# Kernel tuning notes

Measured on AMD Instinct MI355X. Metric: run time of the kernel, lower is better.

Reference implementation:

```python
import jax, jax.numpy as jnp
import numpy as np

B, S, D_MODEL, H, DK, DV, DOUT = 8, 2048, 1024, 1, 512, 512, 1024
EPS = 1e-6
TEMP = DK ** 0.5


def _ln(x, g, b):
    # LayerNorm over last dim, eps=1e-6, affine
    m = jnp.mean(x, axis=-1, keepdims=True)
    v = jnp.mean((x - m) ** 2, axis=-1, keepdims=True)
    return (x - m) * jax.lax.rsqrt(v + EPS) * g + b


def setup_inputs() -> dict:
    key = jax.random.key(0)
    ks = jax.random.split(key, 16)
    s = 0.02
    return {
        "q": jax.random.normal(ks[0], (B, S, D_MODEL), jnp.float32),
        "k": jax.random.normal(ks[1], (B, S, D_MODEL), jnp.float32),
        "v": jax.random.normal(ks[2], (B, S, D_MODEL), jnp.float32),
        "mask": jnp.ones((B, S, S), jnp.int32),
        "Wq": jax.random.normal(ks[3], (D_MODEL, H * DK), jnp.float32) * s,
        "bq": jnp.zeros((H * DK,), jnp.float32),
        "Wk": jax.random.normal(ks[4], (D_MODEL, H * DK), jnp.float32) * s,
        "bk": jnp.zeros((H * DK,), jnp.float32),
        "Wv": jax.random.normal(ks[5], (D_MODEL, H * DV), jnp.float32) * s,
        "bv": jnp.zeros((H * DV,), jnp.float32),
        "g_q": jnp.ones((H * DK,), jnp.float32),
        "be_q": jnp.zeros((H * DK,), jnp.float32),
        "g_k": jnp.ones((H * DK,), jnp.float32),
        "be_k": jnp.zeros((H * DK,), jnp.float32),
        "g_v": jnp.ones((H * DV,), jnp.float32),
        "be_v": jnp.zeros((H * DV,), jnp.float32),
        "W1": jax.random.normal(ks[6], (H * DV, H * DV), jnp.float32) * s,
        "b1": jnp.zeros((H * DV,), jnp.float32),
        "W2": jax.random.normal(ks[7], (H * DV, DOUT), jnp.float32) * s,
        "b2": jnp.zeros((DOUT,), jnp.float32),
    }


def reference(q, k, v, mask, Wq, bq, Wk, bk, Wv, bv, g_q, be_q, g_k, be_k, g_v, be_v, W1, b1, W2, b2):
    # QKV projections, viewed as (B, S, H, d)
    qp = (q @ Wq + bq).reshape(B, S, H, DK)
    kp = (k @ Wk + bk).reshape(B, S, H, DK)
    vp = (v @ Wv + bv).reshape(B, S, H, DV)
    residual = qp
    # per-(token,head) LayerNorm over last dim (valid only because H == 1 in source)
    qn = jnp.swapaxes(_ln(qp, g_q, be_q), 1, 2)  # (B, H, S, DK)
    kn = jnp.swapaxes(_ln(kp, g_k, be_k), 1, 2)
    vn = jnp.swapaxes(_ln(vp, g_v, be_v), 1, 2)
    # scaled dot-product attention with mask
    scores = jnp.einsum('bhqd,bhkd->bhqk', qn / TEMP, kn)
    scores = jnp.where(mask[:, None, :, :] == 0, -1e9, scores)
    attn = jax.nn.softmax(scores, axis=-1)
    out = jnp.einsum('bhqk,bhkd->bhqd', attn, vn)
    out = jnp.swapaxes(out, 1, 2).reshape(B, S, H * DV)
    # trailing 2-layer MLP
    out = jax.nn.relu(out @ W1 + b1) @ W2 + b2
    return (out, residual, jnp.squeeze(attn))
```

## Files before the change

kernel.cpp:

```cpp
#include <hip/hip_runtime.h>
#include <hip/hip_bf16.h>

typedef __attribute__((ext_vector_type(8))) short short8;
typedef __attribute__((ext_vector_type(4))) short short4v;
typedef __attribute__((ext_vector_type(4))) float f32x4;

#define INV_TEMP 0.044194173824159216f

__device__ __forceinline__ ushort f2bf(float f) {
  unsigned u = __float_as_uint(f);
  unsigned r = (u + 0x7FFFu + ((u >> 16) & 1u)) >> 16;
  return (ushort)r;
}
__device__ __forceinline__ float bf2f(ushort u) {
  union { unsigned i; float f; } x; x.i = ((unsigned)u) << 16; return x.f;
}

__device__ __forceinline__ void gload_lds16(const void* g, void* l) {
  __builtin_amdgcn_global_load_lds(
      (const __attribute__((address_space(1))) unsigned int*)(unsigned long long)(uintptr_t)g,
      (__attribute__((address_space(3))) unsigned int*)(unsigned)(uintptr_t)l,
      16, 0, 0);
}

__global__ __launch_bounds__(256)
void transpose_cvt_all(const float* __restrict__ Wq, const float* __restrict__ Wk,
                       const float* __restrict__ Wv, const float* __restrict__ W1,
                       const float* __restrict__ W2,
                       ushort* __restrict__ Tq, ushort* __restrict__ Tk,
                       ushort* __restrict__ Tv, ushort* __restrict__ T1,
                       ushort* __restrict__ T2) {
  const int z = blockIdx.z;
  const int K = (z < 3) ? 1024 : 512;
  const int N = (z == 4) ? 1024 : 512;
  if (blockIdx.x * 32 >= N || blockIdx.y * 32 >= K) return;
  const float* W = z == 0 ? Wq : (z == 1 ? Wk : (z == 2 ? Wv : (z == 3 ? W1 : W2)));
  ushort* WT = z == 0 ? Tq : (z == 1 ? Tk : (z == 2 ? Tv : (z == 3 ? T1 : T2)));
  __shared__ float tile[32][33];
  const int n0 = blockIdx.x * 32, k0 = blockIdx.y * 32;
  const int tx = threadIdx.x & 31, ty = threadIdx.x >> 5;
  #pragma unroll
  for (int i = ty; i < 32; i += 8)
    tile[i][tx] = W[(long)(k0 + i) * N + n0 + tx];
  __syncthreads();
  #pragma unroll
  for (int i = ty; i < 32; i += 8)
    WT[(long)(n0 + i) * K + k0 + tx] = f2bf(tile[tx][i]);
}

__global__ __launch_bounds__(256)
void transpose_bf16(const ushort* __restrict__ in, ushort* __restrict__ out, int S, int D) {
  __shared__ ushort tile[32][33];
  const ushort* inb = in + (long)blockIdx.z * S * D;
  ushort* outb = out + (long)blockIdx.z * S * D;
  const int d0 = blockIdx.x * 32, s0 = blockIdx.y * 32;
  const int tx = threadIdx.x & 31, ty = threadIdx.x >> 5;
  #pragma unroll
  for (int i = ty; i < 32; i += 8)
    tile[i][tx] = inb[(long)(s0 + i) * D + d0 + tx];
  __syncthreads();
  #pragma unroll
  for (int i = ty; i < 32; i += 8)
    outb[(long)(d0 + i) * S + s0 + tx] = tile[tx][i];
}

__global__ __launch_bounds__(256)
void ln3_kernel(const float* __restrict__ Xq, const ushort* __restrict__ Xk,
                const ushort* __restrict__ Xv,
                const float* __restrict__ gq, const float* __restrict__ beq,
                const float* __restrict__ gk, const float* __restrict__ bek,
                const float* __restrict__ gv, const float* __restrict__ bev,
                ushort* __restrict__ Oq, ushort* __restrict__ Ok, ushort* __restrict__ Ov) {
  const int which = blockIdx.y;
  const float* g = which == 0 ? gq : (which == 1 ? gk : gv);
  const float* be = which == 0 ? beq : (which == 1 ? bek : bev);
  ushort* out = which == 0 ? Oq : (which == 1 ? Ok : Ov);
  const float scale = which == 0 ? INV_TEMP : 1.0f;

  const int row = blockIdx.x * 4 + (threadIdx.x >> 6);
  const int lane = threadIdx.x & 63;
  f32x4 v0, v1;
  if (which == 0) {
    const float* x = Xq + (long)row * 512 + lane * 8;
    v0 = *(const f32x4*)x;
    v1 = *(const f32x4*)(x + 4);
  } else {
    const ushort* x = (which == 1 ? Xk : Xv) + (long)row * 512 + lane * 8;
    short8 vv = *(const short8*)x;
    #pragma unroll
    for (int j = 0; j < 4; j++) { v0[j] = bf2f((ushort)vv[j]); v1[j] = bf2f((ushort)vv[4 + j]); }
  }
  float s = v0[0]+v0[1]+v0[2]+v0[3]+v1[0]+v1[1]+v1[2]+v1[3];
  float ss = v0[0]*v0[0]+v0[1]*v0[1]+v0[2]*v0[2]+v0[3]*v0[3]
           + v1[0]*v1[0]+v1[1]*v1[1]+v1[2]*v1[2]+v1[3]*v1[3];
  #pragma unroll
  for (int off = 32; off; off >>= 1) { s += __shfl_xor(s, off); ss += __shfl_xor(ss, off); }
  const float mean = s * (1.0f/512.0f);
  const float var  = ss * (1.0f/512.0f) - mean*mean;
  const float rs = rsqrtf(var + 1e-6f);
  f32x4 g0 = *(const f32x4*)(g + lane*8);
  f32x4 g1 = *(const f32x4*)(g + lane*8 + 4);
  f32x4 b0 = *(const f32x4*)(be + lane*8);
  f32x4 b1 = *(const f32x4*)(be + lane*8 + 4);
  union { short8 v; ushort u[8]; } o;
  #pragma unroll
  for (int j = 0; j < 4; j++) o.u[j]     = f2bf(((v0[j]-mean)*rs*g0[j] + b0[j]) * scale);
  #pragma unroll
  for (int j = 0; j < 4; j++) o.u[4 + j] = f2bf(((v1[j]-mean)*rs*g1[j] + b1[j]) * scale);
  *(short8*)(out + (long)row * 512 + lane * 8) = o.v;
}

template<int EPI, bool HAS_BIAS, bool OUT_BF16, bool A_F32>
__global__ __launch_bounds__(256)
void gemm_tn_pipe(const void* __restrict__ Av, const ushort* __restrict__ Bt,
                  const float* __restrict__ bias, const int* __restrict__ maskp,
                  float* __restrict__ Cf, ushort* __restrict__ Cb,
                  float* __restrict__ partial,
                  const float* __restrict__ A2, const float* __restrict__ A3,
                  const ushort* __restrict__ Bt2, const ushort* __restrict__ Bt3,
                  const float* __restrict__ bias2, const float* __restrict__ bias3,
                  ushort* __restrict__ Cb2,
                  int M, int N, int K,
                  long sA, long sB, long sC) {
  __shared__ char smem_raw[66048];
  ushort (*As)[128 * 64] = (ushort(*)[128 * 64])smem_raw;
  ushort (*Bs)[128 * 64] = (ushort(*)[128 * 64])(smem_raw + 32768);
  float* zloc = (float*)(smem_raw + 65536);
  float* smf  = (float*)smem_raw;

  const int tid = threadIdx.x;
  const int lane = tid & 63;
  const int wave = tid >> 6;
  const int wr = wave >> 1;
  const int wc = wave & 1;

  const int gx = gridDim.x, gy = gridDim.y;
  int lin = blockIdx.x + gx * (blockIdx.y + gy * blockIdx.z);
  const int nwg = gx * gy * (int)gridDim.z;
  int swz = lin;
  if ((nwg & 7) == 0) {
    const int q8 = nwg >> 3;
    swz = (lin & 7) * q8 + (lin >> 3);
  }
  const int bx = swz % gx;
  const int tmp = swz / gx;
  const int by = tmp % gy;
  const int bz = tmp / gy;

  const long zb = bz;
  const float* Afp;
  const ushort* Bb;
  const float* bias_p = bias;
  if constexpr (EPI == 4) {
    Afp = (bz == 0 ? (const float*)Av : (bz == 1 ? A2 : A3)) + (long)by * 128 * K;
    Bb = (bz == 0 ? Bt : (bz == 1 ? Bt2 : Bt3)) + (long)bx * 128 * K;
    bias_p = bz == 0 ? bias : (bz == 1 ? bias2 : bias3);
  } else {
    Afp = (const float*)Av + zb * sA + (long)by * 128 * K;
    Bb = Bt + zb * sB + (long)bx * 128 * K;
  }
  const ushort* Ab = (const ushort*)Av + zb * sA + (long)by * 128 * K;
  const int rowbase0 = by * 128;
  const int nt = K >> 6;

  if constexpr (EPI == 3) {
    if (tid < 128) {
      float z = 0.f;
      #pragma unroll
      for (int j = 0; j < 16; j++)
        z += partial[((long)(zb * 16 + j)) * 2048 + rowbase0 + tid];
      zloc[tid] = 1.0f / z;
    }
  }

  auto stage = [&](int buf, int t) {
    const long kt = (long)t << 6;
    if constexpr (A_F32) {
      f32x4 a[4][2];
      #pragma unroll
      for (int i = 0; i < 4; i++) {
        const int c = i * 256 + tid;
        const int row = c >> 3, g = c & 7;
        const float* p = Afp + (long)row * K + kt + g * 8;
        a[i][0] = *(const f32x4*)p;
        a[i][1] = *(const f32x4*)(p + 4);
      }
      #pragma unroll
      for (int i = 0; i < 4; i++) {
        const int c = i * 256 + tid;
        const int row = c >> 3, g = c & 7, gsrc = g ^ (row & 7);
        gload_lds16(Bb + (long)row * K + kt + gsrc * 8, (char*)Bs[buf] + c * 16);
      }
      #pragma unroll
      for (int i = 0; i < 4; i++) {
        const int c = i * 256 + tid;
        const int row = c >> 3, g = c & 7;
        union { short8 s; ushort u[8]; } o;
        #pragma unroll
        for (int j = 0; j < 4; j++) { o.u[j] = f2bf(a[i][0][j]); o.u[4 + j] = f2bf(a[i][1][j]); }
        *(short8*)((char*)As[buf] + ((row << 7) | ((g << 4) ^ ((row & 7) << 4)))) = o.s;
      }
      asm volatile("s_waitcnt lgkmcnt(0)" ::: "memory");
    } else {
      #pragma unroll
      for (int i = 0; i < 4; i++) {
        const int c = i * 256 + tid;
        const int row = c >> 3, g = c & 7, gsrc = g ^ (row & 7);
        gload_lds16(Ab + (long)row * K + kt + gsrc * 8, (char*)As[buf] + c * 16);
        gload_lds16(Bb + (long)row * K + kt + gsrc * 8, (char*)Bs[buf] + c * 16);
      }
    }
  };

  f32x4 acc[4][4];
  #pragma unroll
  for (int m = 0; m < 4; m++)
    #pragma unroll
    for (int n = 0; n < 4; n++)
      acc[m][n] = f32x4{0.f, 0.f, 0.f, 0.f};

  stage(0, 0);
  stage(1, 1);

  for (int t = 0; t < nt; ++t) {
    const int buf = t & 1;
    if (t == nt - 1) {
      asm volatile("s_waitcnt vmcnt(0)" ::: "memory");
    } else if constexpr (A_F32) {
      asm volatile("s_waitcnt vmcnt(4)" ::: "memory");
    } else {
      asm volatile("s_waitcnt vmcnt(8)" ::: "memory");
    }
    __builtin_amdgcn_s_barrier();
    __builtin_amdgcn_sched_barrier(0);

    if constexpr (EPI == 3) {
      if ((t >> 3) == bx) {
        #pragma unroll
        for (int e = 0; e < 4; e++) {
          const int c = e * 256 + tid;
          const int row = c >> 3, g = c & 7;
          short8 p8 = *(const short8*)((const char*)As[buf] +
                       ((row << 7) | ((g ^ (row & 7)) << 4)));
          const float iz = zloc[row];
          f32x4 o0, o1;
          #pragma unroll
          for (int jj = 0; jj < 4; jj++) {
            o0[jj] = bf2f((ushort)p8[jj]) * iz;
            o1[jj] = bf2f((ushort)p8[4 + jj]) * iz;
          }
          float* dst = Cf + zb * 4194304L + (long)(rowbase0 + row) * 2048 + (t << 6) + g * 8;
          *(f32x4*)dst = o0;
          *(f32x4*)(dst + 4) = o1;
        }
      }
    }

    #pragma unroll
    for (int ks = 0; ks < 2; ks++) {
      short8 af[4], bfr[4];
      const int kb = ks * 64 + ((lane >> 4) << 4);
      #pragma unroll
      for (int m = 0; m < 4; m++) {
        const int row = wr * 64 + m * 16 + (lane & 15);
        af[m] = *(const short8*)((const char*)As[buf] +
                 ((row << 7) | (kb ^ ((row & 7) << 4))));
      }
      #pragma unroll
      for (int n = 0; n < 4; n++) {
        const int col = wc * 64 + n * 16 + (lane & 15);
        bfr[n] = *(const short8*)((const char*)Bs[buf] +
                  ((col << 7) | (kb ^ ((col & 7) << 4))));
      }
      __builtin_amdgcn_s_setprio(1);
      #pragma unroll
      for (int m = 0; m < 4; m++)
        #pragma unroll
        for (int n = 0; n < 4; n++)
          acc[m][n] = __builtin_amdgcn_mfma_f32_16x16x32_bf16(af[m], bfr[n], acc[m][n], 0, 0, 0);
      __builtin_amdgcn_s_setprio(0);
    }
    __builtin_amdgcn_sched_barrier(0);
    __builtin_amdgcn_s_barrier();
    __builtin_amdgcn_sched_barrier(0);
    if (t + 2 < nt) stage(buf, t + 2);
  }

  const int c_lane = lane & 15;
  const int r_lane = (lane >> 4) << 2;

  if constexpr (EPI == 2) {
    const int r_own = tid >> 2;
    const int cq    = (tid & 3) * 32;
    #pragma unroll
    for (int h = 0; h < 2; h++) {
      __syncthreads();
      if (wr == h) {
        #pragma unroll
        for (int n = 0; n < 4; n++)
          #pragma unroll
          for (int m = 0; m < 4; m++)
            #pragma unroll
            for (int r4 = 0; r4 < 4; r4++)
              smf[(m * 16 + r_lane + r4) * 132 + wc * 64 + n * 16 + c_lane] =
                  acc[m][n][r4];
      }
      __syncthreads();
      const int grow = rowbase0 + h * 64 + r_own;
      const int gcolb = bx * 128 + cq;
      const int* mrow = maskp + zb * 4194304L + (long)grow * 2048 + gcolb;
      ushort* orow = Cb + zb * sC + (long)grow * 2048 + gcolb;
      float rsum = 0.f;
      #pragma unroll
      for (int cc = 0; cc < 4; cc++) {
        f32x4 v0 = *(const f32x4*)&smf[r_own * 132 + cq + cc * 8];
        f32x4 v1 = *(const f32x4*)&smf[r_own * 132 + cq + cc * 8 + 4];
        int4 m0 = *(const int4*)(mrow + cc * 8);
        int4 m1 = *(const int4*)(mrow + cc * 8 + 4);
        float e0 = m0.x ? __expf(v0[0]) : 0.f;
        float e1 = m0.y ? __expf(v0[1]) : 0.f;
        float e2 = m0.z ? __expf(v0[2]) : 0.f;
        float e3 = m0.w ? __expf(v0[3]) : 0.f;
        float e4 = m1.x ? __expf(v1[0]) : 0.f;
        float e5 = m1.y ? __expf(v1[1]) : 0.f;
        float e6 = m1.z ? __expf(v1[2]) : 0.f;
        float e7 = m1.w ? __expf(v1[3]) : 0.f;
        rsum += (e0 + e1 + e2 + e3) + (e4 + e5 + e6 + e7);
        union { short8 s; ushort u[8]; } o;
        o.u[0] = f2bf(e0); o.u[1] = f2bf(e1); o.u[2] = f2bf(e2); o.u[3] = f2bf(e3);
        o.u[4] = f2bf(e4); o.u[5] = f2bf(e5); o.u[6] = f2bf(e6); o.u[7] = f2bf(e7);
        *(short8*)(orow + cc * 8) = o.s;
      }
      rsum += __shfl_xor(rsum, 1);
      rsum += __shfl_xor(rsum, 2);
      if ((tid & 3) == 0)
        partial[((long)zb * 16 + bx) * 2048 + grow] = rsum;
    }
  } else {
    const int colbase = bx * 128 + wc * 64;
    const int rowbase = by * 128 + wr * 64;
    #pragma unroll
    for (int n = 0; n < 4; n++) {
      const int col = colbase + n * 16 + c_lane;
      const float bv = HAS_BIAS ? bias_p[col] : 0.0f;
      #pragma unroll
      for (int m = 0; m < 4; m++) {
        const int rbase = rowbase + m * 16 + r_lane;
        #pragma unroll
        for (int r4 = 0; r4 < 4; r4++) {
          const int row = rbase + r4;
          float vv = acc[m][n][r4] + bv;
          if constexpr (EPI == 1) vv = fmaxf(vv, 0.0f);
          if constexpr (EPI == 3) vv *= zloc[wr * 64 + m * 16 + r_lane + r4];
          const long off = zb * sC + (long)row * N + col;
          if constexpr (EPI == 4) {
            if (bz == 0) Cf[off] = vv;
            else if (bz == 1) Cb[off] = f2bf(vv);
            else Cb2[off] = f2bf(vv);
          } else if constexpr (OUT_BF16) {
            Cb[off] = f2bf(vv);
          } else {
            Cf[off] = vv;
          }
        }
      }
    }
  }
}

extern "C" void kernel_launch(void* const* d_in, const int* in_sizes, int n_in,
                              void* d_out, int out_size, void* d_ws, size_t ws_size,
                              hipStream_t stream) {
  const float* q    = (const float*)d_in[0];
  const float* k    = (const float*)d_in[1];
  const float* v    = (const float*)d_in[2];
  const int*   mask = (const int*)d_in[3];
  const float* Wq   = (const float*)d_in[4];
  const float* bq   = (const float*)d_in[5];
  const float* Wk   = (const float*)d_in[6];
  const float* bk   = (const float*)d_in[7];
  const float* Wv   = (const float*)d_in[8];
  const float* bv   = (const float*)d_in[9];
  const float* g_q  = (const float*)d_in[10];
  const float* be_q = (const float*)d_in[11];
  const float* g_k  = (const float*)d_in[12];
  const float* be_k = (const float*)d_in[13];
  const float* g_v  = (const float*)d_in[14];
  const float* be_v = (const float*)d_in[15];
  const float* W1   = (const float*)d_in[16];
  const float* b1   = (const float*)d_in[17];
  const float* W2   = (const float*)d_in[18];
  const float* b2   = (const float*)d_in[19];

  float* out_mlp  = (float*)d_out;
  float* out_res  = out_mlp + 16777216L;
  float* out_attn = out_res + 8388608L;

  char* w = (char*)d_ws;
  ushort* qn      = (ushort*)(w);
  ushort* kn      = (ushort*)(w + 16777216UL);
  ushort* kp_bf   = (ushort*)(w + 33554432UL);
  ushort* vp_bf   = (ushort*)(w + 50331648UL);
  ushort* attn_bf = (ushort*)(w + 33554432UL);
  ushort* vn      = (ushort*)(w + 100663296UL);
  ushort* vnT     = (ushort*)(w + 117440512UL);
  ushort* pv      = (ushort*)(w + 134217728UL);
  ushort* h       = (ushort*)(w + 150994944UL);
  ushort* wqT     = (ushort*)(w + 167772160UL);
  ushort* wkT     = (ushort*)(w + 168820736UL);
  ushort* wvT     = (ushort*)(w + 169869312UL);
  ushort* w1T     = (ushort*)(w + 170917888UL);
  ushort* w2T     = (ushort*)(w + 171442176UL);
  float*  partial = (float*)(w + 172490752UL);

  dim3 blk(256);

  transpose_cvt_all<<<dim3(32, 32, 5), blk, 0, stream>>>(
      Wq, Wk, Wv, W1, W2, wqT, wkT, wvT, w1T, w2T);

  gemm_tn_pipe<4, true, false, true><<<dim3(4, 128, 3), blk, 0, stream>>>(
      q, wqT, bq, nullptr, out_res, kp_bf, nullptr,
      k, v, wkT, wvT, bk, bv, vp_bf,
      16384, 512, 1024, 0, 0, 0);

  ln3_kernel<<<dim3(4096, 3), blk, 0, stream>>>(
      out_res, kp_bf, vp_bf, g_q, be_q, g_k, be_k, g_v, be_v, qn, kn, vn);

  transpose_bf16<<<dim3(16, 64, 8), blk, 0, stream>>>(vn, vnT, 2048, 512);

  gemm_tn_pipe<2, false, true, false><<<dim3(16, 16, 8), blk, 0, stream>>>(
      qn, kn, nullptr, mask, nullptr, attn_bf, partial,
      nullptr, nullptr, nullptr, nullptr, nullptr, nullptr, nullptr,
      2048, 2048, 512,
      (long)2048 * 512, (long)2048 * 512, (long)2048 * 2048);

  gemm_tn_pipe<3, false, true, false><<<dim3(4, 16, 8), blk, 0, stream>>>(
      attn_bf, vnT, nullptr, nullptr, out_attn, pv, partial,
      nullptr, nullptr, nullptr, nullptr, nullptr, nullptr, nullptr,
      2048, 512, 2048,
      (long)2048 * 2048, (long)512 * 2048, (long)2048 * 512);

  gemm_tn_pipe<1, true, true, false><<<dim3(4, 128, 1), blk, 0, stream>>>(
      pv, w1T, b1, nullptr, nullptr, h, nullptr,
      nullptr, nullptr, nullptr, nullptr, nullptr, nullptr, nullptr,
      16384, 512, 512, 0, 0, 0);
  gemm_tn_pipe<0, true, false, false><<<dim3(8, 128, 1), blk, 0, stream>>>(
      h, w2T, b2, nullptr, out_mlp, nullptr, nullptr,
      nullptr, nullptr, nullptr, nullptr, nullptr, nullptr, nullptr,
      16384, 1024, 512, 0, 0, 0);
}
```

Baseline: 352.5 us.

## Add dedicated 256x256-tile scores GEMM kernel with 512 threads and prefetched mask

Replaces the 128x128-tile QK^T scores GEMM (EPI==2 path) with a dedicated kernel that uses 256x256 output tiles, 8 waves, 128KB LDS double buffering, and loads the mask ahead of the epilogue's LDS staging. Larger tiles halve the global reloads of Q and K per output element and halve the number of row-sum partials, so the PV kernel now reduces 8 partials instead of 16. The cost is heavy LDS use and high register pressure (32 accumulators per thread), which limits occupancy to one block per CU, and a 512-block grid that may leave some CUs unevenly loaded.

```diff
diff --git a/kernel.cpp b/kernel.cpp
--- a/kernel.cpp
+++ b/kernel.cpp
@@ -110,10 +110,154 @@
   *(short8*)(out + (long)row * 512 + lane * 8) = o.v;
 }
 
+__global__ __launch_bounds__(512)
+void gemm_scores256(const ushort* __restrict__ qn, const ushort* __restrict__ kn,
+                    const int* __restrict__ maskp, ushort* __restrict__ Cb,
+                    float* __restrict__ partial) {
+  __shared__ char smem_raw[131072];
+  ushort (*As)[16384] = (ushort(*)[16384])smem_raw;
+  ushort (*Bs)[16384] = (ushort(*)[16384])(smem_raw + 65536);
+  float* smf = (float*)smem_raw;
+
+  const int tid = threadIdx.x;
+  const int lane = tid & 63;
+  const int wave = tid >> 6;
+  const int wr = wave >> 2;
+  const int wc = wave & 3;
+
+  int lin = blockIdx.x + 8 * (blockIdx.y + 8 * blockIdx.z);
+  const int q8 = 64;
+  const int swz = (lin & 7) * q8 + (lin >> 3);
+  const int bx = swz & 7;
+  const int by = (swz >> 3) & 7;
+  const int bz = swz >> 6;
+
+  const long zb = bz;
+  const ushort* Ab = qn + zb * (2048L * 512) + (long)by * 256 * 512;
+  const ushort* Bb = kn + zb * (2048L * 512) + (long)bx * 256 * 512;
+  const int nt = 8;
+
+  auto stage = [&](int buf, int t) {
+    const long kt = (long)t << 6;
+    #pragma unroll
+    for (int i = 0; i < 4; i++) {
+      const int c = i * 512 + tid;
+      const int row = c >> 3, g = c & 7, gsrc = g ^ (row & 7);
+      gload_lds16(Ab + (long)row * 512 + kt + gsrc * 8, (char*)As[buf] + c * 16);
+      gload_lds16(Bb + (long)row * 512 + kt + gsrc * 8, (char*)Bs[buf] + c * 16);
+    }
+  };
+
+  f32x4 acc[8][4];
+  #pragma unroll
+  for (int m = 0; m < 8; m++)
+    #pragma unroll
+    for (int n = 0; n < 4; n++)
+      acc[m][n] = f32x4{0.f, 0.f, 0.f, 0.f};
+
+  stage(0, 0);
+  stage(1, 1);
+
+  for (int t = 0; t < nt; ++t) {
+    const int buf = t & 1;
+    if (t == nt - 1) {
+      asm volatile("s_waitcnt vmcnt(0)" ::: "memory");
+    } else {
+      asm volatile("s_waitcnt vmcnt(8)" ::: "memory");
+    }
+    __builtin_amdgcn_s_barrier();
+    __builtin_amdgcn_sched_barrier(0);
+
+    #pragma unroll
+    for (int ks = 0; ks < 2; ks++) {
+      short8 af[8], bfr[4];
+      const int kb = ks * 64 + ((lane >> 4) << 4);
+      #pragma unroll
+      for (int m = 0; m < 8; m++) {
+        const int row = wr * 128 + m * 16 + (lane & 15);
+        af[m] = *(const short8*)((const char*)As[buf] +
+                 ((row << 7) | (kb ^ ((row & 7) << 4))));
+      }
+      #pragma unroll
+      for (int n = 0; n < 4; n++) {
+        const int col = wc * 64 + n * 16 + (lane & 15);
+        bfr[n] = *(const short8*)((const char*)Bs[buf] +
+                  ((col << 7) | (kb ^ ((col & 7) << 4))));
+      }
+      __builtin_amdgcn_s_setprio(1);
+      #pragma unroll
+      for (int m = 0; m < 8; m++)
+        #pragma unroll
+        for (int n = 0; n < 4; n++)
+          acc[m][n] = __builtin_amdgcn_mfma_f32_16x16x32_bf16(af[m], bfr[n], acc[m][n], 0, 0, 0);
+      __builtin_amdgcn_s_setprio(0);
+    }
+    __builtin_amdgcn_sched_barrier(0);
+    __builtin_amdgcn_s_barrier();
+    __builtin_amdgcn_sched_barrier(0);
+    if (t + 2 < nt) stage(buf, t + 2);
+  }
+
+  const int c_lane = lane & 15;
+  const int r_lane = (lane >> 4) << 2;
+  const int r_own = tid >> 3;
+  const int cq = (tid & 7) * 32;
+  #pragma unroll
+  for (int p = 0; p < 4; p++) {
+    const int grow = by * 256 + p * 64 + r_own;
+    const int gcol = bx * 256 + cq;
+    const int* mrow = maskp + zb * 4194304L + (long)grow * 2048 + gcol;
+    int4 mk[8];
+    #pragma unroll
+    for (int cc = 0; cc < 8; cc++) mk[cc] = *(const int4*)(mrow + cc * 4);
+
+    __syncthreads();
+    if (wr == (p >> 1)) {
+      const int mbase = (p & 1) * 4;
+      #pragma unroll
+      for (int mm = 0; mm < 4; mm++)
+        #pragma unroll
+        for (int n = 0; n < 4; n++)
+          #pragma unroll
+          for (int r4 = 0; r4 < 4; r4++)
+            smf[(mm * 16 + r_lane + r4) * 260 + wc * 64 + n * 16 + c_lane] =
+                acc[mbase + mm][n][r4];
+    }
+    __syncthreads();
+
+    ushort* orow = Cb + zb * 4194304L + (long)grow * 2048 + gcol;
+    float rsum = 0.f;
+    #pragma unroll
+    for (int cc = 0; cc < 4; cc++) {
+      f32x4 v0 = *(const f32x4*)&smf[r_own * 260 + cq + cc * 8];
+      f32x4 v1 = *(const f32x4*)&smf[r_own * 260 + cq + cc * 8 + 4];
+      int4 m0 = mk[cc * 2], m1 = mk[cc * 2 + 1];
+      float e0 = m0.x ? __expf(v0[0]) : 0.f;
+      float e1 = m0.y ? __expf(v0[1]) : 0.f;
+      float e2 = m0.z ? __expf(v0[2]) : 0.f;
+      float e3 = m0.w ? __expf(v0[3]) : 0.f;
+      float e4 = m1.x ? __expf(v1[0]) : 0.f;
+      float e5 = m1.y ? __expf(v1[1]) : 0.f;
+      float e6 = m1.z ? __expf(v1[2]) : 0.f;
+      float e7 = m1.w ? __expf(v1[3]) : 0.f;
+      rsum += (e0 + e1 + e2 + e3) + (e4 + e5 + e6 + e7);
+      union { short8 s; ushort u[8]; } o;
+      o.u[0] = f2bf(e0); o.u[1] = f2bf(e1); o.u[2] = f2bf(e2); o.u[3] = f2bf(e3);
+      o.u[4] = f2bf(e4); o.u[5] = f2bf(e5); o.u[6] = f2bf(e6); o.u[7] = f2bf(e7);
+      *(short8*)(orow + cc * 8) = o.s;
+    }
+    rsum += __shfl_xor(rsum, 1);
+    rsum += __shfl_xor(rsum, 2);
+    rsum += __shfl_xor(rsum, 4);
+    if ((tid & 7) == 0)
+      partial[((long)zb * 8 + bx) * 2048 + grow] = rsum;
+  }
+}
+
 template<int EPI, bool HAS_BIAS, bool OUT_BF16, bool A_F32>
 __global__ __launch_bounds__(256)
 void gemm_tn_pipe(const void* __restrict__ Av, const ushort* __restrict__ Bt,
-                  const float* __restrict__ bias, const int* __restrict__ maskp,
+                  const float* __restrict__ bias,
                   float* __restrict__ Cf, ushort* __restrict__ Cb,
                   float* __restrict__ partial,
                   const float* __restrict__ A2, const float* __restrict__ A3,
@@ -126,7 +270,6 @@
   ushort (*As)[128 * 64] = (ushort(*)[128 * 64])smem_raw;
   ushort (*Bs)[128 * 64] = (ushort(*)[128 * 64])(smem_raw + 32768);
   float* zloc = (float*)(smem_raw + 65536);
-  float* smf  = (float*)smem_raw;
 
   const int tid = threadIdx.x;
   const int lane = tid & 63;
@@ -167,8 +310,8 @@
     if (tid < 128) {
       float z = 0.f;
       #pragma unroll
-      for (int j = 0; j < 16; j++)
-        z += partial[((long)(zb * 16 + j)) * 2048 + rowbase0 + tid];
+      for (int j = 0; j < 8; j++)
+        z += partial[((long)(zb * 8 + j)) * 2048 + rowbase0 + tid];
       zloc[tid] = 1.0f / z;
     }
   }
@@ -288,80 +431,30 @@
 
   const int c_lane = lane & 15;
   const int r_lane = (lane >> 4) << 2;
-
-  if constexpr (EPI == 2) {
-    const int r_own = tid >> 2;
-    const int cq    = (tid & 3) * 32;
-    #pragma unroll
-    for (int h = 0; h < 2; h++) {
-      __syncthreads();
-      if (wr == h) {
-        #pragma unroll
-        for (int n = 0; n < 4; n++)
-          #pragma unroll
-          for (int m = 0; m < 4; m++)
-            #pragma unroll
-            for (int r4 = 0; r4 < 4; r4++)
-              smf[(m * 16 + r_lane + r4) * 132 + wc * 64 + n * 16 + c_lane] =
-                  acc[m][n][r4];
-      }
-      __syncthreads();
-      const int grow = rowbase0 + h * 64 + r_own;
-      const int gcolb = bx * 128 + cq;
-      const int* mrow = maskp + zb * 4194304L + (long)grow * 2048 + gcolb;
-      ushort* orow = Cb + zb * sC + (long)grow * 2048 + gcolb;
-      float rsum = 0.f;
-      #pragma unroll
-      for (int cc = 0; cc < 4; cc++) {
-        f32x4 v0 = *(const f32x4*)&smf[r_own * 132 + cq + cc * 8];
-        f32x4 v1 = *(const f32x4*)&smf[r_own * 132 + cq + cc * 8 + 4];
-        int4 m0 = *(const int4*)(mrow + cc * 8);
-        int4 m1 = *(const int4*)(mrow + cc * 8 + 4);
-        float e0 = m0.x ? __expf(v0[0]) : 0.f;
-        float e1 = m0.y ? __expf(v0[1]) : 0.f;
-        float e2 = m0.z ? __expf(v0[2]) : 0.f;
-        float e3 = m0.w ? __expf(v0[3]) : 0.f;
-        float e4 = m1.x ? __expf(v1[0]) : 0.f;
-        float e5 = m1.y ? __expf(v1[1]) : 0.f;
-        float e6 = m1.z ? __expf(v1[2]) : 0.f;
-        float e7 = m1.w ? __expf(v1[3]) : 0.f;
-        rsum += (e0 + e1 + e2 + e3) + (e4 + e5 + e6 + e7);
-        union { short8 s; ushort u[8]; } o;
-        o.u[0] = f2bf(e0); o.u[1] = f2bf(e1); o.u[2] = f2bf(e2); o.u[3] = f2bf(e3);
-        o.u[4] = f2bf(e4); o.u[5] = f2bf(e5); o.u[6] = f2bf(e6); o.u[7] = f2bf(e7);
-        *(short8*)(orow + cc * 8) = o.s;
-      }
-      rsum += __shfl_xor(rsum, 1);
-      rsum += __shfl_xor(rsum, 2);
-      if ((tid & 3) == 0)
-        partial[((long)zb * 16 + bx) * 2048 + grow] = rsum;
-    }
-  } else {
-    const int colbase = bx * 128 + wc * 64;
-    const int rowbase = by * 128 + wr * 64;
-    #pragma unroll
-    for (int n = 0; n < 4; n++) {
-      const int col = colbase + n * 16 + c_lane;
-      const float bv = HAS_BIAS ? bias_p[col] : 0.0f;
-      #pragma unroll
-      for (int m = 0; m < 4; m++) {
-        const int rbase = rowbase + m * 16 + r_lane;
-        #pragma unroll
-        for (int r4 = 0; r4 < 4; r4++) {
-          const int row = rbase + r4;
-          float vv = acc[m][n][r4] + bv;
-          if constexpr (EPI == 1) vv = fmaxf(vv, 0.0f);
-          if constexpr (EPI == 3) vv *= zloc[wr * 64 + m * 16 + r_lane + r4];
-          const long off = zb * sC + (long)row * N + col;
-          if constexpr (EPI == 4) {
-            if (bz == 0) Cf[off] = vv;
-            else if (bz == 1) Cb[off] = f2bf(vv);
-            else Cb2[off] = f2bf(vv);
-          } else if constexpr (OUT_BF16) {
-            Cb[off] = f2bf(vv);
-          } else {
-            Cf[off] = vv;
-          }
+  const int colbase = bx * 128 + wc * 64;
+  const int rowbase = by * 128 + wr * 64;
+  #pragma unroll
+  for (int n = 0; n < 4; n++) {
+    const int col = colbase + n * 16 + c_lane;
+    const float bv = HAS_BIAS ? bias_p[col] : 0.0f;
+    #pragma unroll
+    for (int m = 0; m < 4; m++) {
+      const int rbase = rowbase + m * 16 + r_lane;
+      #pragma unroll
+      for (int r4 = 0; r4 < 4; r4++) {
+        const int row = rbase + r4;
+        float vv = acc[m][n][r4] + bv;
+        if constexpr (EPI == 1) vv = fmaxf(vv, 0.0f);
+        if constexpr (EPI == 3) vv *= zloc[wr * 64 + m * 16 + r_lane + r4];
+        const long off = zb * sC + (long)row * N + col;
+        if constexpr (EPI == 4) {
+          if (bz == 0) Cf[off] = vv;
+          else if (bz == 1) Cb[off] = f2bf(vv);
+          else Cb2[off] = f2bf(vv);
+        } else if constexpr (OUT_BF16) {
+          Cb[off] = f2bf(vv);
+        } else {
+          Cf[off] = vv;
         }
       }
     }
@@ -419,7 +512,7 @@
       Wq, Wk, Wv, W1, W2, wqT, wkT, wvT, w1T, w2T);
 
   gemm_tn_pipe<4, true, false, true><<<dim3(4, 128, 3), blk, 0, stream>>>(
-      q, wqT, bq, nullptr, out_res, kp_bf, nullptr,
+      q, wqT, bq, out_res, kp_bf, nullptr,
       k, v, wkT, wvT, bk, bv, vp_bf,
       16384, 512, 1024, 0, 0, 0);
 
@@ -428,24 +521,21 @@
 
   transpose_bf16<<<dim3(16, 64, 8), blk, 0, stream>>>(vn, vnT, 2048, 512);
 
-  gemm_tn_pipe<2, false, true, false><<<dim3(16, 16, 8), blk, 0, stream>>>(
-      qn, kn, nullptr, mask, nullptr, attn_bf, partial,
-      nullptr, nullptr, nullptr, nullptr, nullptr, nullptr, nullptr,
-      2048, 2048, 512,
-      (long)2048 * 512, (long)2048 * 512, (long)2048 * 2048);
+  gemm_scores256<<<dim3(8, 8, 8), dim3(512), 0, stream>>>(
+      qn, kn, mask, attn_bf, partial);
 
   gemm_tn_pipe<3, false, true, false><<<dim3(4, 16, 8), blk, 0, stream>>>(
-      attn_bf, vnT, nullptr, nullptr, out_attn, pv, partial,
+      attn_bf, vnT, nullptr, out_attn, pv, partial,
       nullptr, nullptr, nullptr, nullptr, nullptr, nullptr, nullptr,
       2048, 512, 2048,
       (long)2048 * 2048, (long)512 * 2048, (long)2048 * 512);
 
   gemm_tn_pipe<1, true, true, false><<<dim3(4, 128, 1), blk, 0, stream>>>(
-      pv, w1T, b1, nullptr, nullptr, h, nullptr,
+      pv, w1T, b1, nullptr, h, nullptr,
       nullptr, nullptr, nullptr, nullptr, nullptr, nullptr, nullptr,
       16384, 512, 512, 0, 0, 0);
   gemm_tn_pipe<0, true, false, false><<<dim3(8, 128, 1), blk, 0, stream>>>(
-      h, w2T, b2, nullptr, out_mlp, nullptr, nullptr,
+      h, w2T, b2, out_mlp, nullptr, nullptr,
       nullptr, nullptr, nullptr, nullptr, nullptr, nullptr, nullptr,
       16384, 1024, 512, 0, 0, 0);
 }
```

Result: no change. 355.7 us (+0.9%).
